# Performance work log

Measured on AMD Instinct MI355X. Metric: run time of the kernel, lower is better.

Reference implementation:

```python
import jax, jax.numpy as jnp
import numpy as np

D_MODEL = 1024
N_HEADS = 16
HEAD_DIM = D_MODEL // N_HEADS  # 64; used only as softmax scale in windowed path
WINDOW = 128


def _window_starts(seq_len, window):
    # Faithful to the torch loop: stride = window//2, last window right-aligned.
    starts = []
    for i in range(0, seq_len, window // 2):
        end = min(i + window, seq_len)
        starts.append(max(0, end - window))
        if end == seq_len:
            break
    return np.asarray(starts, dtype=np.int32)


def setup_inputs() -> dict:
    key = jax.random.key(0)
    ks = jax.random.split(key, 9)
    B, S = 4, 4096
    sc = 1.0 / np.sqrt(D_MODEL)
    return {
        "x": jax.random.normal(ks[0], (B, S, D_MODEL), jnp.float32),
        "Wq": jax.random.normal(ks[1], (D_MODEL, D_MODEL), jnp.float32) * sc,
        "bq": jax.random.normal(ks[2], (D_MODEL,), jnp.float32) * 0.02,
        "Wk": jax.random.normal(ks[3], (D_MODEL, D_MODEL), jnp.float32) * sc,
        "bk": jax.random.normal(ks[4], (D_MODEL,), jnp.float32) * 0.02,
        "Wv": jax.random.normal(ks[5], (D_MODEL, D_MODEL), jnp.float32) * sc,
        "bv": jax.random.normal(ks[6], (D_MODEL,), jnp.float32) * 0.02,
        "Wo": jax.random.normal(ks[7], (D_MODEL, D_MODEL), jnp.float32) * sc,
        "bo": jax.random.normal(ks[8], (D_MODEL,), jnp.float32) * 0.02,
    }


def reference(x, Wq, bq, Wk, bk, Wv, bv, Wo, bo):
    B, S, D = x.shape
    q = x @ Wq + bq  # [B,S,D]
    k = x @ Wk + bk
    v = x @ Wv + bv

    # Overlapping sliding windows (heads merged, as in the original windowed path).
    starts = _window_starts(S, WINDOW)                      # [W]
    idx = starts[:, None] + np.arange(WINDOW)[None, :]      # [W, w] static
    idx_j = jnp.asarray(idx)
    qw = q[:, idx_j]  # [B, W, w, D]
    kw = k[:, idx_j]
    vw = v[:, idx_j]
    scores = jnp.einsum('bwqd,bwkd->bwqk', qw, kw) / np.sqrt(HEAD_DIM)
    attn = jax.nn.softmax(scores, axis=-1)
    out_w = jnp.einsum('bwqk,bwkd->bwqd', attn, vw)         # [B, W, w, D]

    # Overlap-add then average by coverage counts.
    flat_idx = idx.reshape(-1)
    out = jnp.zeros((B, S, D), x.dtype).at[:, flat_idx].add(
        out_w.reshape(B, -1, D))
    counts = jnp.zeros((S,), x.dtype).at[flat_idx].add(1.0)
    out = out / counts[None, :, None]

    return out @ Wo + bo
```

## Files before the change

### kernel.cpp

```cpp
#include <hip/hip_runtime.h>
#include <stdint.h>
#include <stddef.h>

#define D_MODEL 1024
#define SEQ     4096
#define BATCH   4
#define MTOT    (BATCH*SEQ)
#define NWIN    63

typedef __bf16 bf16;
typedef __bf16 bf16x8 __attribute__((ext_vector_type(8)));
typedef __bf16 bf16x4 __attribute__((ext_vector_type(4)));
typedef float  floatx4 __attribute__((ext_vector_type(4)));

__device__ __forceinline__ void async_ld16(const void* g, void* l) {
  __builtin_amdgcn_global_load_lds(
      (const __attribute__((address_space(1))) unsigned int*)g,
      (__attribute__((address_space(3))) unsigned int*)l,
      16, 0, 0);
}


__global__ __launch_bounds__(256)
void cvt_x_kernel(const float* __restrict__ x, bf16* __restrict__ xb)
{
  const int i = blockIdx.x * 256 + threadIdx.x;
  const float4 v = ((const float4*)x)[i];
  bf16x4 o = { (bf16)v.x, (bf16)v.y, (bf16)v.z, (bf16)v.w };
  ((bf16x4*)xb)[i] = o;
}

__global__ __launch_bounds__(256)
void cvt_wt_kernel(const float* __restrict__ W0, const float* __restrict__ W1,
                   const float* __restrict__ W2, const float* __restrict__ W3,
                   bf16* __restrict__ wt)
{
  __shared__ float tile[32][33];
  const float* Wsel = (blockIdx.z == 0) ? W0 : (blockIdx.z == 1) ? W1
                    : (blockIdx.z == 2) ? W2 : W3;
  bf16* Wt = wt + (size_t)blockIdx.z * D_MODEL * D_MODEL;
  const int tx = threadIdx.x & 31, ty = threadIdx.x >> 5;
  const int tn = blockIdx.x * 32, tk = blockIdx.y * 32;
#pragma unroll
  for (int j = 0; j < 32; j += 8)
    tile[ty + j][tx] = Wsel[(size_t)(tk + ty + j) * D_MODEL + (tn + tx)];
  __syncthreads();
#pragma unroll
  for (int j = 0; j < 32; j += 8)
    Wt[(size_t)(tn + ty + j) * D_MODEL + (tk + tx)] = (bf16)tile[tx][ty + j];
}

__device__ __forceinline__ void gemm_core_pipe(const bf16* __restrict__ A,
                                               const bf16* __restrict__ Bt,
                                               int Kdim, int m0, int n0,
                                               bf16* As, bf16* Bs,
                                               floatx4 (&acc)[4][4],
                                               int w, int l)
{
  const int ll = l & 15, lh = l >> 4;
  const int wm = w >> 1, wn = w & 1;

  bf16x8 ar[4], br[4];

  auto load_regs = [&](int k0) {
#pragma unroll
    for (int i = 0; i < 4; ++i) {
      const int f = w * 4 + i;
      const int mt = f & 7, kk = f >> 3;
      ar[i] = *(const bf16x8*)(A  + (size_t)(m0 + mt * 16 + ll) * Kdim + (k0 + kk * 32 + lh * 8));
      br[i] = *(const bf16x8*)(Bt + (size_t)(n0 + mt * 16 + ll) * Kdim + (k0 + kk * 32 + lh * 8));
    }
  };
  auto store_lds = [&](int buf) {
    bf16* Ad = As + buf * 8192;
    bf16* Bd = Bs + buf * 8192;
#pragma unroll
    for (int i = 0; i < 4; ++i) {
      const int f = w * 4 + i;
      *(bf16x8*)&Ad[f * 512 + l * 8] = ar[i];
      *(bf16x8*)&Bd[f * 512 + l * 8] = br[i];
    }
  };

  load_regs(0);
  store_lds(0);
  __syncthreads();

  const int T = Kdim >> 6;
  for (int t = 0; t < T; ++t) {
    if (t + 1 < T) load_regs((t + 1) << 6);
    const bf16* Ac = As + (t & 1) * 8192;
    const bf16* Bc = Bs + (t & 1) * 8192;
#pragma unroll
    for (int kk = 0; kk < 2; ++kk) {
      bf16x8 af[4], bfr[4];
#pragma unroll
      for (int tt = 0; tt < 4; ++tt) {
        af[tt]  = *(const bf16x8*)&Ac[(kk * 8 + wm * 4 + tt) * 512 + l * 8];
        bfr[tt] = *(const bf16x8*)&Bc[(kk * 8 + wn * 4 + tt) * 512 + l * 8];
      }
#pragma unroll
      for (int mt = 0; mt < 4; ++mt)
#pragma unroll
        for (int nt = 0; nt < 4; ++nt)
          acc[mt][nt] = __builtin_amdgcn_mfma_f32_16x16x32_bf16(af[mt], bfr[nt], acc[mt][nt], 0, 0, 0);
    }
    if (t + 1 < T) store_lds((t + 1) & 1);
    __syncthreads();
  }
}

__global__ __launch_bounds__(256)
void gemm_qkv(const bf16* __restrict__ A, const bf16* __restrict__ Bt,
              const float* __restrict__ bq, const float* __restrict__ bk,
              const float* __restrict__ bv,
              bf16* __restrict__ qo, bf16* __restrict__ ko, bf16* __restrict__ vto)
{
  __shared__ __attribute__((aligned(16))) bf16 As[16384];
  __shared__ __attribute__((aligned(16))) bf16 Bs[16384];
  const int tid = threadIdx.x;
  const int w = tid >> 6, l = tid & 63;
  const int ll = l & 15, lh = l >> 4;
  const int wm = w >> 1, wn = w & 1;

  const int idx = blockIdx.x;
  const int xcd = idx & 7;
  const int local = idx >> 3;
  const int msub = local & 3;
  const int nblk = (local >> 2) % 24;
  const int sub  = local / 96;
  const int mblk = xcd * 16 + sub * 4 + msub;
  const int m0 = mblk * 128, n0 = nblk * 128;

  floatx4 acc[4][4];
#pragma unroll
  for (int i = 0; i < 4; ++i)
#pragma unroll
    for (int j = 0; j < 4; ++j) acc[i][j] = (floatx4)0.f;

  gemm_core_pipe(A, Bt, D_MODEL, m0, n0, As, Bs, acc, w, l);

  const int sel = n0 >> 10;
  const int ncl = n0 & 1023;
  const float* bias = (sel == 0) ? bq : (sel == 1) ? bk : bv;

#pragma unroll
  for (int mt = 0; mt < 4; ++mt) {
#pragma unroll
    for (int nt = 0; nt < 4; ++nt) {
      const int colL = ncl + wn * 64 + nt * 16 + ll;
      const float bvv = bias[colL];
#pragma unroll
      for (int r = 0; r < 4; ++r) {
        const int row = m0 + wm * 64 + mt * 16 + lh * 4 + r;
        const float v = acc[mt][nt][r] + bvv;
        if (sel == 0) {
          qo[(size_t)row * D_MODEL + colL] = (bf16)v;
        } else if (sel == 1) {
          ko[(size_t)row * D_MODEL + colL] = (bf16)v;
        } else {
          const int bb = row >> 12, s = row & 4095;
          vto[((size_t)bb * D_MODEL + colL) * SEQ + s] = (bf16)v;
        }
      }
    }
  }
}

__global__ __launch_bounds__(256)
void gemm_out(const bf16* __restrict__ A, const bf16* __restrict__ Bt,
              const float* __restrict__ bias, float* __restrict__ C)
{
  __shared__ __attribute__((aligned(16))) bf16 As[16384];
  __shared__ __attribute__((aligned(16))) bf16 Bs[16384];
  const int tid = threadIdx.x;
  const int w = tid >> 6, l = tid & 63;
  const int ll = l & 15, lh = l >> 4;
  const int wm = w >> 1, wn = w & 1;

  const int idx = blockIdx.x;
  const int xcd = idx & 7;
  const int local = idx >> 3;
  const int msub = local & 3;
  const int nblk = (local >> 2) & 7;
  const int sub  = local >> 5;
  const int mblk = xcd * 16 + sub * 4 + msub;
  const int m0 = mblk * 128, n0 = nblk * 128;

  floatx4 acc[4][4];
#pragma unroll
  for (int i = 0; i < 4; ++i)
#pragma unroll
    for (int j = 0; j < 4; ++j) acc[i][j] = (floatx4)0.f;

  gemm_core_pipe(A, Bt, D_MODEL, m0, n0, As, Bs, acc, w, l);

#pragma unroll
  for (int mt = 0; mt < 4; ++mt) {
#pragma unroll
    for (int nt = 0; nt < 4; ++nt) {
      const int col = n0 + wn * 64 + nt * 16 + ll;
      const float bvv = bias[col];
#pragma unroll
      for (int r = 0; r < 4; ++r) {
        const int row = m0 + wm * 64 + mt * 16 + lh * 4 + r;
        C[(size_t)row * D_MODEL + col] = acc[mt][nt][r] + bvv;
      }
    }
  }
}

__global__ __launch_bounds__(256)
void qk_softmax(const bf16* __restrict__ qb, const bf16* __restrict__ kb,
                bf16* __restrict__ Pg)
{
  __shared__ __attribute__((aligned(16))) bf16 As[8192];
  __shared__ __attribute__((aligned(16))) bf16 Bs[16384];
  __shared__ float redM[4][64];
  __shared__ float redS[4][64];

  const int tid = threadIdx.x;
  const int w = tid >> 6, l = tid & 63, ll = l & 15, lh = l >> 4;
  const int wh = blockIdx.x;
  const int win = wh >> 1, half = wh & 1;
  const int b = blockIdx.y;

  const bf16* Aq = qb + ((size_t)b * SEQ + win * 64 + half * 64) * D_MODEL;
  const bf16* Ak = kb + ((size_t)b * SEQ + win * 64) * D_MODEL;

  floatx4 acc[4][2];
#pragma unroll
  for (int i = 0; i < 4; ++i)
#pragma unroll
    for (int j = 0; j < 2; ++j) acc[i][j] = (floatx4)0.f;

  bf16x8 qr[2], kr[4];

  auto load_regs = [&](int c0) {
#pragma unroll
    for (int i = 0; i < 2; ++i) {
      const int f = w * 2 + i;
      const int mt = f & 3, kk = f >> 2;
      qr[i] = *(const bf16x8*)(Aq + (size_t)(mt * 16 + ll) * D_MODEL + (c0 + kk * 32 + lh * 8));
    }
#pragma unroll
    for (int i = 0; i < 4; ++i) {
      const int f = w * 4 + i;
      const int mt = f & 7, kk = f >> 3;
      kr[i] = *(const bf16x8*)(Ak + (size_t)(mt * 16 + ll) * D_MODEL + (c0 + kk * 32 + lh * 8));
    }
  };
  auto store_lds = [&](int buf) {
    bf16* Ad = As + buf * 4096;
    bf16* Bd = Bs + buf * 8192;
#pragma unroll
    for (int i = 0; i < 2; ++i) {
      const int f = w * 2 + i;
      *(bf16x8*)&Ad[f * 512 + l * 8] = qr[i];
    }
#pragma unroll
    for (int i = 0; i < 4; ++i) {
      const int f = w * 4 + i;
      *(bf16x8*)&Bd[f * 512 + l * 8] = kr[i];
    }
  };

  load_regs(0);
  store_lds(0);
  __syncthreads();

  for (int t = 0; t < 16; ++t) {
    if (t + 1 < 16) load_regs((t + 1) << 6);
    const bf16* Ac = As + (t & 1) * 4096;
    const bf16* Bc = Bs + (t & 1) * 8192;
#pragma unroll
    for (int kk = 0; kk < 2; ++kk) {
      bf16x8 af[4], bfr[2];
#pragma unroll
      for (int tt = 0; tt < 4; ++tt)
        af[tt]  = *(const bf16x8*)&Ac[(kk * 4 + tt) * 512 + l * 8];
#pragma unroll
      for (int tt = 0; tt < 2; ++tt)
        bfr[tt] = *(const bf16x8*)&Bc[(kk * 8 + w * 2 + tt) * 512 + l * 8];
#pragma unroll
      for (int mt = 0; mt < 4; ++mt)
#pragma unroll
        for (int nt = 0; nt < 2; ++nt)
          acc[mt][nt] = __builtin_amdgcn_mfma_f32_16x16x32_bf16(af[mt], bfr[nt], acc[mt][nt], 0, 0, 0);
    }
    if (t + 1 < 16) store_lds((t + 1) & 1);
    __syncthreads();
  }

#pragma unroll
  for (int mt = 0; mt < 4; ++mt)
#pragma unroll
    for (int nt = 0; nt < 2; ++nt)
#pragma unroll
      for (int r = 0; r < 4; ++r) acc[mt][nt][r] *= 0.125f;

#pragma unroll
  for (int mt = 0; mt < 4; ++mt)
#pragma unroll
    for (int r = 0; r < 4; ++r) {
      float m = fmaxf(acc[mt][0][r], acc[mt][1][r]);
      m = fmaxf(m, __shfl_xor(m, 1));
      m = fmaxf(m, __shfl_xor(m, 2));
      m = fmaxf(m, __shfl_xor(m, 4));
      m = fmaxf(m, __shfl_xor(m, 8));
      if (ll == 0) redM[w][mt * 16 + lh * 4 + r] = m;
    }
  __syncthreads();

#pragma unroll
  for (int mt = 0; mt < 4; ++mt)
#pragma unroll
    for (int r = 0; r < 4; ++r) {
      const int row = mt * 16 + lh * 4 + r;
      const float m = fmaxf(fmaxf(redM[0][row], redM[1][row]),
                            fmaxf(redM[2][row], redM[3][row]));
      const float e0 = __expf(acc[mt][0][r] - m);
      const float e1 = __expf(acc[mt][1][r] - m);
      acc[mt][0][r] = e0; acc[mt][1][r] = e1;
      float s = e0 + e1;
      s += __shfl_xor(s, 1);
      s += __shfl_xor(s, 2);
      s += __shfl_xor(s, 4);
      s += __shfl_xor(s, 8);
      if (ll == 0) redS[w][row] = s;
    }
  __syncthreads();

  bf16* Pb = Pg + ((size_t)(b * NWIN + win) * 128 + half * 64) * 128;
#pragma unroll
  for (int mt = 0; mt < 4; ++mt)
#pragma unroll
    for (int r = 0; r < 4; ++r) {
      const int row = mt * 16 + lh * 4 + r;
      const float inv = 1.f / (redS[0][row] + redS[1][row] + redS[2][row] + redS[3][row]);
#pragma unroll
      for (int nt = 0; nt < 2; ++nt)
        Pb[(size_t)row * 128 + w * 32 + nt * 16 + ll] = (bf16)(acc[mt][nt][r] * inv);
    }
}

__global__ __launch_bounds__(256)
void pv_gather(const bf16* __restrict__ Pg, const bf16* __restrict__ vt,
               bf16* __restrict__ ab)
{
  __shared__ __attribute__((aligned(16))) bf16 As[4096];
  __shared__ __attribute__((aligned(16))) bf16 Bs[8192];

  const int tid = threadIdx.x;
  const int w = tid >> 6, l = tid & 63, ll = l & 15, lh = l >> 4;
  const int d0 = blockIdx.x * 128;
  const int h  = blockIdx.y;
  const int b  = blockIdx.z;

  int wseg[2], roff[2];
  int nseg = 0;
  if (h >= 1)        { wseg[nseg] = h - 1; roff[nseg] = 64; ++nseg; }
  if (h <= NWIN - 1) { wseg[nseg] = h;     roff[nseg] = 0;  ++nseg; }
  const float scale = (nseg == 2) ? 0.5f : 1.0f;

  floatx4 acc[4][2];
#pragma unroll
  for (int i = 0; i < 4; ++i)
#pragma unroll
    for (int j = 0; j < 2; ++j) acc[i][j] = (floatx4)0.f;

  for (int sg = 0; sg < nseg; ++sg) {
    const bf16* Pseg = Pg + ((size_t)(b * NWIN + wseg[sg]) * 128 + roff[sg]) * 128;
    const bf16* Vseg = vt + ((size_t)b * D_MODEL + d0) * SEQ + wseg[sg] * 64;
    for (int c0 = 0; c0 < 128; c0 += 64) {
#pragma unroll
      for (int i = 0; i < 2; ++i) {
        const int f = w * 2 + i;
        const int mt = f & 3, kk = f >> 2;
        async_ld16(Pseg + (size_t)(mt * 16 + ll) * 128 + (c0 + kk * 32 + lh * 8),
                   &As[f * 512 + l * 8]);
      }
#pragma unroll
      for (int i = 0; i < 4; ++i) {
        const int f = w * 4 + i;
        const int mt = f & 7, kk = f >> 3;
        async_ld16(Vseg + (size_t)(mt * 16 + ll) * SEQ + (c0 + kk * 32 + lh * 8),
                   &Bs[f * 512 + l * 8]);
      }
      __syncthreads();
#pragma unroll
      for (int kk = 0; kk < 2; ++kk) {
        bf16x8 af[4], bfr[2];
#pragma unroll
        for (int t = 0; t < 4; ++t)
          af[t]  = *(const bf16x8*)&As[(kk * 4 + t) * 512 + l * 8];
#pragma unroll
        for (int t = 0; t < 2; ++t)
          bfr[t] = *(const bf16x8*)&Bs[(kk * 8 + w * 2 + t) * 512 + l * 8];
#pragma unroll
        for (int mt = 0; mt < 4; ++mt)
#pragma unroll
          for (int nt = 0; nt < 2; ++nt)
            acc[mt][nt] = __builtin_amdgcn_mfma_f32_16x16x32_bf16(af[mt], bfr[nt], acc[mt][nt], 0, 0, 0);
      }
      __syncthreads();
    }
  }

#pragma unroll
  for (int mt = 0; mt < 4; ++mt)
#pragma unroll
    for (int nt = 0; nt < 2; ++nt)
#pragma unroll
      for (int r = 0; r < 4; ++r) {
        const int row = h * 64 + mt * 16 + lh * 4 + r;
        const int col = d0 + w * 32 + nt * 16 + ll;
        ab[((size_t)b * SEQ + row) * D_MODEL + col] = (bf16)(acc[mt][nt][r] * scale);
      }
}

extern "C" void kernel_launch(void* const* d_in, const int* in_sizes, int n_in,
                              void* d_out, int out_size, void* d_ws, size_t ws_size,
                              hipStream_t stream)
{
  (void)in_sizes; (void)n_in; (void)out_size;

  const float* x  = (const float*)d_in[0];
  const float* Wq = (const float*)d_in[1];
  const float* bq = (const float*)d_in[2];
  const float* Wk = (const float*)d_in[3];
  const float* bk = (const float*)d_in[4];
  const float* Wv = (const float*)d_in[5];
  const float* bv = (const float*)d_in[6];
  const float* Wo = (const float*)d_in[7];
  const float* bo = (const float*)d_in[8];

  if (ws_size < (size_t)176160768) return;
  char* ws = (char*)d_ws;
  bf16* xb = (bf16*)(ws);
  bf16* pb = (bf16*)(ws);
  bf16* wt = (bf16*)(ws + 33554432);
  bf16* qb = (bf16*)(ws + 41943040);
  bf16* kb = (bf16*)(ws + 75497472);
  bf16* vt = (bf16*)(ws + 109051904);
  bf16* ab = (bf16*)(ws + 142606336);

  cvt_x_kernel<<<16384, 256, 0, stream>>>(x, xb);
  cvt_wt_kernel<<<dim3(32, 32, 4), 256, 0, stream>>>(Wq, Wk, Wv, Wo, wt);

  gemm_qkv<<<3072, 256, 0, stream>>>(xb, wt, bq, bk, bv, qb, kb, vt);

  qk_softmax<<<dim3(126, BATCH), 256, 0, stream>>>(qb, kb, pb);
  pv_gather<<<dim3(8, 64, BATCH), 256, 0, stream>>>(pb, vt, ab);

  gemm_out<<<1024, 256, 0, stream>>>(ab, wt + 3145728, bo, (float*)d_out);
}
```

Baseline: 498.3 us.

## Replace register-staged double-buffered GEMM loads with direct global-to-LDS single buffer

The GEMM cores and the QK/softmax kernel now move tiles from global memory straight into LDS with global_load_lds, instead of loading into registers and storing to LDS. LDS drops from double to single buffering, with a barrier before and after each k-step. This removes register staging and cuts LDS use, which may allow higher occupancy. The cost is that loads no longer overlap with MFMA compute inside a block, so latency hiding depends on other resident blocks. The code also relies on __syncthreads alone to wait for the async LDS loads, which may be a correctness risk.

```diff
diff --git a/kernel.cpp b/kernel.cpp
--- a/kernel.cpp
+++ b/kernel.cpp
@@ -50,54 +50,38 @@
     Wt[(size_t)(tn + ty + j) * D_MODEL + (tk + tx)] = (bf16)tile[tx][ty + j];
 }
 
-__device__ __forceinline__ void gemm_core_pipe(const bf16* __restrict__ A,
-                                               const bf16* __restrict__ Bt,
-                                               int Kdim, int m0, int n0,
-                                               bf16* As, bf16* Bs,
-                                               floatx4 (&acc)[4][4],
-                                               int w, int l)
+__device__ __forceinline__ void gemm_core_lds(const bf16* __restrict__ A,
+                                              const bf16* __restrict__ Bt,
+                                              int m0, int n0,
+                                              bf16* As, bf16* Bs,
+                                              floatx4 (&acc)[4][4],
+                                              int w, int l)
 {
   const int ll = l & 15, lh = l >> 4;
   const int wm = w >> 1, wn = w & 1;
 
-  bf16x8 ar[4], br[4];
-
-  auto load_regs = [&](int k0) {
+  const bf16* Abase = A  + (size_t)(m0 + ll) * D_MODEL + lh * 8;
+  const bf16* Bbase = Bt + (size_t)(n0 + ll) * D_MODEL + lh * 8;
+
+  for (int t = 0; t < 16; ++t) {
+    const int k0 = t << 6;
 #pragma unroll
     for (int i = 0; i < 4; ++i) {
       const int f = w * 4 + i;
       const int mt = f & 7, kk = f >> 3;
-      ar[i] = *(const bf16x8*)(A  + (size_t)(m0 + mt * 16 + ll) * Kdim + (k0 + kk * 32 + lh * 8));
-      br[i] = *(const bf16x8*)(Bt + (size_t)(n0 + mt * 16 + ll) * Kdim + (k0 + kk * 32 + lh * 8));
-    }
-  };
-  auto store_lds = [&](int buf) {
-    bf16* Ad = As + buf * 8192;
-    bf16* Bd = Bs + buf * 8192;
-#pragma unroll
-    for (int i = 0; i < 4; ++i) {
-      const int f = w * 4 + i;
-      *(bf16x8*)&Ad[f * 512 + l * 8] = ar[i];
-      *(bf16x8*)&Bd[f * 512 + l * 8] = br[i];
-    }
-  };
-
-  load_regs(0);
-  store_lds(0);
-  __syncthreads();
-
-  const int T = Kdim >> 6;
-  for (int t = 0; t < T; ++t) {
-    if (t + 1 < T) load_regs((t + 1) << 6);
-    const bf16* Ac = As + (t & 1) * 8192;
-    const bf16* Bc = Bs + (t & 1) * 8192;
+      async_ld16(Abase + (size_t)(mt * 16) * D_MODEL + (k0 + kk * 32),
+                 &As[f * 512 + l * 8]);
+      async_ld16(Bbase + (size_t)(mt * 16) * D_MODEL + (k0 + kk * 32),
+                 &Bs[f * 512 + l * 8]);
+    }
+    __syncthreads();
 #pragma unroll
     for (int kk = 0; kk < 2; ++kk) {
       bf16x8 af[4], bfr[4];
 #pragma unroll
       for (int tt = 0; tt < 4; ++tt) {
-        af[tt]  = *(const bf16x8*)&Ac[(kk * 8 + wm * 4 + tt) * 512 + l * 8];
-        bfr[tt] = *(const bf16x8*)&Bc[(kk * 8 + wn * 4 + tt) * 512 + l * 8];
+        af[tt]  = *(const bf16x8*)&As[(kk * 8 + wm * 4 + tt) * 512 + l * 8];
+        bfr[tt] = *(const bf16x8*)&Bs[(kk * 8 + wn * 4 + tt) * 512 + l * 8];
       }
 #pragma unroll
       for (int mt = 0; mt < 4; ++mt)
@@ -105,7 +89,6 @@
         for (int nt = 0; nt < 4; ++nt)
           acc[mt][nt] = __builtin_amdgcn_mfma_f32_16x16x32_bf16(af[mt], bfr[nt], acc[mt][nt], 0, 0, 0);
     }
-    if (t + 1 < T) store_lds((t + 1) & 1);
     __syncthreads();
   }
 }
@@ -116,8 +99,8 @@
               const float* __restrict__ bv,
               bf16* __restrict__ qo, bf16* __restrict__ ko, bf16* __restrict__ vto)
 {
-  __shared__ __attribute__((aligned(16))) bf16 As[16384];
-  __shared__ __attribute__((aligned(16))) bf16 Bs[16384];
+  __shared__ __attribute__((aligned(16))) bf16 As[8192];
+  __shared__ __attribute__((aligned(16))) bf16 Bs[8192];
   const int tid = threadIdx.x;
   const int w = tid >> 6, l = tid & 63;
   const int ll = l & 15, lh = l >> 4;
@@ -138,7 +121,7 @@
 #pragma unroll
     for (int j = 0; j < 4; ++j) acc[i][j] = (floatx4)0.f;
 
-  gemm_core_pipe(A, Bt, D_MODEL, m0, n0, As, Bs, acc, w, l);
+  gemm_core_lds(A, Bt, m0, n0, As, Bs, acc, w, l);
 
   const int sel = n0 >> 10;
   const int ncl = n0 & 1023;
@@ -171,8 +154,8 @@
 void gemm_out(const bf16* __restrict__ A, const bf16* __restrict__ Bt,
               const float* __restrict__ bias, float* __restrict__ C)
 {
-  __shared__ __attribute__((aligned(16))) bf16 As[16384];
-  __shared__ __attribute__((aligned(16))) bf16 Bs[16384];
+  __shared__ __attribute__((aligned(16))) bf16 As[8192];
+  __shared__ __attribute__((aligned(16))) bf16 Bs[8192];
   const int tid = threadIdx.x;
   const int w = tid >> 6, l = tid & 63;
   const int ll = l & 15, lh = l >> 4;
@@ -193,7 +176,7 @@
 #pragma unroll
     for (int j = 0; j < 4; ++j) acc[i][j] = (floatx4)0.f;
 
-  gemm_core_pipe(A, Bt, D_MODEL, m0, n0, As, Bs, acc, w, l);
+  gemm_core_lds(A, Bt, m0, n0, As, Bs, acc, w, l);
 
 #pragma unroll
   for (int mt = 0; mt < 4; ++mt) {
@@ -214,8 +197,8 @@
 void qk_softmax(const bf16* __restrict__ qb, const bf16* __restrict__ kb,
                 bf16* __restrict__ Pg)
 {
-  __shared__ __attribute__((aligned(16))) bf16 As[8192];
-  __shared__ __attribute__((aligned(16))) bf16 Bs[16384];
+  __shared__ __attribute__((aligned(16))) bf16 As[4096];
+  __shared__ __attribute__((aligned(16))) bf16 Bs[8192];
   __shared__ float redM[4][64];
   __shared__ float redS[4][64];
 
@@ -225,8 +208,10 @@
   const int win = wh >> 1, half = wh & 1;
   const int b = blockIdx.y;
 
-  const bf16* Aq = qb + ((size_t)b * SEQ + win * 64 + half * 64) * D_MODEL;
-  const bf16* Ak = kb + ((size_t)b * SEQ + win * 64) * D_MODEL;
+  const bf16* Aq = qb + ((size_t)b * SEQ + win * 64 + half * 64) * D_MODEL
+                 + (size_t)ll * D_MODEL + lh * 8;
+  const bf16* Ak = kb + ((size_t)b * SEQ + win * 64) * D_MODEL
+                 + (size_t)ll * D_MODEL + lh * 8;
 
   floatx4 acc[4][2];
 #pragma unroll
@@ -234,61 +219,38 @@
 #pragma unroll
     for (int j = 0; j < 2; ++j) acc[i][j] = (floatx4)0.f;
 
-  bf16x8 qr[2], kr[4];
-
-  auto load_regs = [&](int c0) {
+  for (int t = 0; t < 16; ++t) {
+    const int c0 = t << 6;
 #pragma unroll
     for (int i = 0; i < 2; ++i) {
       const int f = w * 2 + i;
       const int mt = f & 3, kk = f >> 2;
-      qr[i] = *(const bf16x8*)(Aq + (size_t)(mt * 16 + ll) * D_MODEL + (c0 + kk * 32 + lh * 8));
+      async_ld16(Aq + (size_t)(mt * 16) * D_MODEL + (c0 + kk * 32),
+                 &As[f * 512 + l * 8]);
     }
 #pragma unroll
     for (int i = 0; i < 4; ++i) {
       const int f = w * 4 + i;
       const int mt = f & 7, kk = f >> 3;
-      kr[i] = *(const bf16x8*)(Ak + (size_t)(mt * 16 + ll) * D_MODEL + (c0 + kk * 32 + lh * 8));
-    }
-  };
-  auto store_lds = [&](int buf) {
-    bf16* Ad = As + buf * 4096;
-    bf16* Bd = Bs + buf * 8192;
-#pragma unroll
-    for (int i = 0; i < 2; ++i) {
-      const int f = w * 2 + i;
-      *(bf16x8*)&Ad[f * 512 + l * 8] = qr[i];
-    }
-#pragma unroll
-    for (int i = 0; i < 4; ++i) {
-      const int f = w * 4 + i;
-      *(bf16x8*)&Bd[f * 512 + l * 8] = kr[i];
-    }
-  };
-
-  load_regs(0);
-  store_lds(0);
-  __syncthreads();
-
-  for (int t = 0; t < 16; ++t) {
-    if (t + 1 < 16) load_regs((t + 1) << 6);
-    const bf16* Ac = As + (t & 1) * 4096;
-    const bf16* Bc = Bs + (t & 1) * 8192;
+      async_ld16(Ak + (size_t)(mt * 16) * D_MODEL + (c0 + kk * 32),
+                 &Bs[f * 512 + l * 8]);
+    }
+    __syncthreads();
 #pragma unroll
     for (int kk = 0; kk < 2; ++kk) {
       bf16x8 af[4], bfr[2];
 #pragma unroll
       for (int tt = 0; tt < 4; ++tt)
-        af[tt]  = *(const bf16x8*)&Ac[(kk * 4 + tt) * 512 + l * 8];
+        af[tt]  = *(const bf16x8*)&As[(kk * 4 + tt) * 512 + l * 8];
 #pragma unroll
       for (int tt = 0; tt < 2; ++tt)
-        bfr[tt] = *(const bf16x8*)&Bc[(kk * 8 + w * 2 + tt) * 512 + l * 8];
+        bfr[tt] = *(const bf16x8*)&Bs[(kk * 8 + w * 2 + tt) * 512 + l * 8];
 #pragma unroll
       for (int mt = 0; mt < 4; ++mt)
 #pragma unroll
         for (int nt = 0; nt < 2; ++nt)
           acc[mt][nt] = __builtin_amdgcn_mfma_f32_16x16x32_bf16(af[mt], bfr[nt], acc[mt][nt], 0, 0, 0);
     }
-    if (t + 1 < 16) store_lds((t + 1) & 1);
     __syncthreads();
   }
 
```

Result: no change. 494.5 us (-0.8%).
